# Kernel tuning notes

Hardware: AMD Instinct MI355X
Metric: run time of the kernel (lower is better)

The kernel has to match this reference:

```python
import jax, jax.numpy as jnp
import numpy as np

FP8_MAX = 448.0  # float8_e4m3fn max
EPS = 1e-6


def _rms_norm(x, w):
    # x: [T, H], w: [H]
    var = jnp.mean(x * x, axis=-1, keepdims=True)
    return x * jax.lax.rsqrt(var + EPS) * w


def _fused_add_rms_norm(x, resid, w):
    r = x + resid
    return _rms_norm(r, w), r


def _fp8_linear(y, W):
    # dynamic per-token activation quant + per-tensor weight quant, fp8 e4m3
    s = jnp.maximum(jnp.max(jnp.abs(y), axis=-1, keepdims=True) / FP8_MAX, 1e-12)  # [T,1]
    qx = jnp.clip(y / s, -FP8_MAX, FP8_MAX).astype(jnp.float8_e4m3fn).astype(jnp.float32)
    ws = jnp.maximum(jnp.max(jnp.abs(W)) / FP8_MAX, 1e-12)  # scalar
    qw = jnp.clip(W / ws, -FP8_MAX, FP8_MAX).astype(jnp.float8_e4m3fn).astype(jnp.float32)
    # out = dequant(qx) @ dequant(qw).T = (qx @ qw.T) * s * ws ; W is [out, in]
    return (qx @ qw.T) * (s * ws)


def setup_inputs() -> dict:
    key = jax.random.key(0)
    ks = jax.random.split(key, 8)
    H, T = 4096, 4096
    x = jax.random.normal(ks[0], (T, H), dtype=jnp.float32)
    nw0 = 1.0 + 0.02 * jax.random.normal(ks[1], (H,), dtype=jnp.float32)
    nw1 = 1.0 + 0.02 * jax.random.normal(ks[2], (H,), dtype=jnp.float32)
    nw2 = 1.0 + 0.02 * jax.random.normal(ks[3], (H,), dtype=jnp.float32)
    nw3 = 1.0 + 0.02 * jax.random.normal(ks[4], (H,), dtype=jnp.float32)
    W0 = 0.02 * jax.random.normal(ks[5], (H, H), dtype=jnp.float32)
    W1 = 0.02 * jax.random.normal(ks[6], (H, H), dtype=jnp.float32)
    W2 = 0.02 * jax.random.normal(ks[7], (H, H), dtype=jnp.float32)
    return {"x": x, "nw0": nw0, "nw1": nw1, "nw2": nw2, "nw3": nw3,
            "W0": W0, "W1": W1, "W2": W2}


def reference(x, nw0, nw1, nw2, nw3, W0, W1, W2):
    x = jax.nn.relu(x)
    resid = x
    y = _rms_norm(x, nw0)
    x2 = _fp8_linear(y, W0)
    y2, resid = _fused_add_rms_norm(x2, resid, nw1)
    x3 = _fp8_linear(y2, W1)
    y3, resid = _fused_add_rms_norm(x3, resid, nw2)
    x4 = _fp8_linear(y3, W2)
    y4, resid = _fused_add_rms_norm(x4, resid, nw3)
    return y4
```

## Files before the change

### kernel.cpp

```cpp
#include <hip/hip_runtime.h>
#include <cstdint>
#include <cstddef>

#define AS1 __attribute__((address_space(1)))
#define AS3 __attribute__((address_space(3)))

typedef __attribute__((ext_vector_type(4))) float f32x4;
typedef __attribute__((ext_vector_type(16))) float f32x16;
typedef __attribute__((ext_vector_type(4))) int i32x4;
typedef __attribute__((ext_vector_type(8))) int i32x8;

constexpr int HD = 4096;
constexpr float FP8MAX = 448.0f;

__device__ inline uint32_t pack4_fp8(float a, float b, float c, float d) {
    int v = 0;
    v = __builtin_amdgcn_cvt_pk_fp8_f32(a, b, v, false);
    v = __builtin_amdgcn_cvt_pk_fp8_f32(c, d, v, true);
    return (uint32_t)v;
}

__device__ inline float clipmul(float y, float rcs) {
    float t = y * rcs;
    t = fminf(t, FP8MAX);
    t = fmaxf(t, -FP8MAX);
    return t;
}

__device__ inline uint32_t quant4(float4 v, float rcs) {
    return pack4_fp8(clipmul(v.x, rcs), clipmul(v.y, rcs),
                     clipmul(v.z, rcs), clipmul(v.w, rcs));
}

__device__ inline float max4(float4 v) {
    return fmaxf(fmaxf(fabsf(v.x), fabsf(v.y)), fmaxf(fabsf(v.z), fabsf(v.w)));
}

__global__ __launch_bounds__(256) void w_absmax(const float* __restrict__ W0,
                                                const float* __restrict__ W1,
                                                const float* __restrict__ W2,
                                                uint32_t* __restrict__ wmax) {
    __shared__ float red[4];
    const float* W = (blockIdx.z == 0) ? W0 : (blockIdx.z == 1 ? W1 : W2);
    const float4* W4 = (const float4*)W;
    const int n4 = HD * HD / 4;
    float m = 0.f;
    for (int i = blockIdx.x * blockDim.x + threadIdx.x; i < n4; i += gridDim.x * blockDim.x) {
        m = fmaxf(m, max4(W4[i]));
    }
#pragma unroll
    for (int i = 32; i > 0; i >>= 1) m = fmaxf(m, __shfl_xor(m, i, 64));
    if ((threadIdx.x & 63) == 0) red[threadIdx.x >> 6] = m;
    __syncthreads();
    if (threadIdx.x == 0) {
        m = fmaxf(fmaxf(red[0], red[1]), fmaxf(red[2], red[3]));
        atomicMax((unsigned int*)(wmax + blockIdx.z), __float_as_uint(m));
    }
}

__global__ __launch_bounds__(256) void w_absmax1(const float* __restrict__ W,
                                                 uint32_t* __restrict__ slot) {
    __shared__ float red[4];
    const float4* W4 = (const float4*)W;
    const int stride = 2048 * 256;
    int i = blockIdx.x * 256 + threadIdx.x;
    float a0 = 0.f, a1 = 0.f, a2 = 0.f, a3 = 0.f;
#pragma unroll
    for (int it = 0; it < 2; it++) {
        float4 v0 = W4[i];
        float4 v1 = W4[i + stride];
        float4 v2 = W4[i + 2 * stride];
        float4 v3 = W4[i + 3 * stride];
        a0 = fmaxf(a0, max4(v0));
        a1 = fmaxf(a1, max4(v1));
        a2 = fmaxf(a2, max4(v2));
        a3 = fmaxf(a3, max4(v3));
        i += 4 * stride;
    }
    float m = fmaxf(fmaxf(a0, a1), fmaxf(a2, a3));
#pragma unroll
    for (int s = 32; s > 0; s >>= 1) m = fmaxf(m, __shfl_xor(m, s, 64));
    if ((threadIdx.x & 63) == 0) red[threadIdx.x >> 6] = m;
    __syncthreads();
    if (threadIdx.x == 0) {
        m = fmaxf(fmaxf(red[0], red[1]), fmaxf(red[2], red[3]));
        atomicMax((unsigned int*)slot, __float_as_uint(m));
    }
}

__global__ __launch_bounds__(256) void w_quant(const float* __restrict__ W,
                                               const uint32_t* __restrict__ wmaxbits,
                                               uint32_t* __restrict__ qw) {
    const float rsw = 1.0f / fmaxf(__uint_as_float(*wmaxbits) / FP8MAX, 1e-12f);
    const int i = blockIdx.x * blockDim.x + threadIdx.x;
    qw[i] = quant4(((const float4*)W)[i], rsw);
}

__global__ __launch_bounds__(256) void fused_rms(const float* __restrict__ xin,
                                                 const float* __restrict__ addin,
                                                 float* __restrict__ resid_out,
                                                 const float* __restrict__ nw,
                                                 uint32_t* __restrict__ qx,
                                                 float* __restrict__ srow,
                                                 float* __restrict__ yout,
                                                 const int mode,
                                                 const float* __restrict__ Wq,
                                                 const uint32_t* __restrict__ wqmaxbits,
                                                 uint32_t* __restrict__ qwout,
                                                 const float* __restrict__ Wa1,
                                                 const float* __restrict__ Wa2,
                                                 uint32_t* __restrict__ wmaxbase) {
    const int tid = threadIdx.x;
    __shared__ float reds[4];
    __shared__ float redm[4];

    if (blockIdx.x >= 8192) {
        const int b = blockIdx.x - 8192;
        const float* W = (b < 512) ? Wa1 : Wa2;
        uint32_t* slot = wmaxbase + ((b < 512) ? 1 : 2);
        const int bb = b & 511;
        const float4* W4 = (const float4*)W;
        const int stride = 512 * 256;
        int i = bb * 256 + tid;
        float a0 = 0.f, a1 = 0.f, a2 = 0.f, a3 = 0.f;
#pragma unroll
        for (int it = 0; it < 8; it++) {
            float4 v0 = W4[i];
            float4 v1 = W4[i + stride];
            float4 v2 = W4[i + 2 * stride];
            float4 v3 = W4[i + 3 * stride];
            a0 = fmaxf(a0, max4(v0));
            a1 = fmaxf(a1, max4(v1));
            a2 = fmaxf(a2, max4(v2));
            a3 = fmaxf(a3, max4(v3));
            i += 4 * stride;
        }
        float m = fmaxf(fmaxf(a0, a1), fmaxf(a2, a3));
#pragma unroll
        for (int s = 32; s > 0; s >>= 1) m = fmaxf(m, __shfl_xor(m, s, 64));
        if ((tid & 63) == 0) reds[tid >> 6] = m;
        __syncthreads();
        if (tid == 0) {
            m = fmaxf(fmaxf(reds[0], reds[1]), fmaxf(reds[2], reds[3]));
            atomicMax((unsigned int*)slot, __float_as_uint(m));
        }
        return;
    }

    if (blockIdx.x >= 4096) {
        const float rsw = 1.0f / fmaxf(__uint_as_float(*wqmaxbits) / FP8MAX, 1e-12f);
        const float4* W4 = (const float4*)Wq;
        int i = (blockIdx.x - 4096) * 256 + tid;
#pragma unroll
        for (int it = 0; it < 4; it++, i += 4096 * 256)
            qwout[i] = quant4(W4[i], rsw);
        return;
    }

    const int row = blockIdx.x;
    const size_t base = (size_t)row * HD;
    const float4* xr = (const float4*)(xin + base);
    const float4* nw4 = (const float4*)nw;

    float4 v[4], w[4];
    float ss = 0.f, pm = 0.f;
    if (mode == 0) {
#pragma unroll
        for (int j = 0; j < 4; j++) {
            float4 t = xr[tid + j * 256];
            w[j] = nw4[tid + j * 256];
            t.x = fmaxf(t.x, 0.f); t.y = fmaxf(t.y, 0.f);
            t.z = fmaxf(t.z, 0.f); t.w = fmaxf(t.w, 0.f);
            v[j] = t;
            ss += t.x * t.x + t.y * t.y + t.z * t.z + t.w * t.w;
            pm = fmaxf(pm, fmaxf(fmaxf(fabsf(t.x * w[j].x), fabsf(t.y * w[j].y)),
                                 fmaxf(fabsf(t.z * w[j].z), fabsf(t.w * w[j].w))));
        }
    } else {
        const float4* ar = (const float4*)(addin + base);
#pragma unroll
        for (int j = 0; j < 4; j++) {
            float4 t = xr[tid + j * 256];
            float4 a = ar[tid + j * 256];
            w[j] = nw4[tid + j * 256];
            t.x += a.x; t.y += a.y; t.z += a.z; t.w += a.w;
            v[j] = t;
            ss += t.x * t.x + t.y * t.y + t.z * t.z + t.w * t.w;
            pm = fmaxf(pm, fmaxf(fmaxf(fabsf(t.x * w[j].x), fabsf(t.y * w[j].y)),
                                 fmaxf(fabsf(t.z * w[j].z), fabsf(t.w * w[j].w))));
        }
    }
    if (resid_out) {
        float4* ro = (float4*)(resid_out + base);
#pragma unroll
        for (int j = 0; j < 4; j++) ro[tid + j * 256] = v[j];
    }

#pragma unroll
    for (int i = 32; i > 0; i >>= 1) {
        ss += __shfl_xor(ss, i, 64);
        pm = fmaxf(pm, __shfl_xor(pm, i, 64));
    }
    if ((tid & 63) == 0) { reds[tid >> 6] = ss; redm[tid >> 6] = pm; }
    __syncthreads();
    ss = (reds[0] + reds[1]) + (reds[2] + reds[3]);
    pm = fmaxf(fmaxf(redm[0], redm[1]), fmaxf(redm[2], redm[3]));

    const float rs = 1.0f / sqrtf(ss / (float)HD + 1e-6f);

    if (mode == 2) {
        float4* yo = (float4*)(yout + base);
#pragma unroll
        for (int j = 0; j < 4; j++) {
            float4 t;
            t.x = (v[j].x * rs) * w[j].x; t.y = (v[j].y * rs) * w[j].y;
            t.z = (v[j].z * rs) * w[j].z; t.w = (v[j].w * rs) * w[j].w;
            yo[tid + j * 256] = t;
        }
        return;
    }

    const float amax = pm * rs;
    const float s = fmaxf(amax / FP8MAX, 1e-12f);
    const float rcs = 1.0f / s;
    if (tid == 0) srow[row] = s;
    uint32_t* qr = qx + base / 4;
#pragma unroll
    for (int j = 0; j < 4; j++) {
        float4 t;
        t.x = (v[j].x * rs) * w[j].x; t.y = (v[j].y * rs) * w[j].y;
        t.z = (v[j].z * rs) * w[j].z; t.w = (v[j].w * rs) * w[j].w;
        qr[tid + j * 256] = quant4(t, rcs);
    }
}

typedef union { i32x8 v8; i32x4 v4[2]; } frag8;

__global__ __launch_bounds__(512, 2) void gemm_fp8mx(const uint8_t* __restrict__ qx,
                                                     const uint8_t* __restrict__ qw,
                                                     const float* __restrict__ srow,
                                                     const uint32_t* __restrict__ wmaxbits,
                                                     float* __restrict__ out) {
    __shared__ i32x4 AsL[2][2][1024];
    __shared__ i32x4 BsL[2][2][1024];

    const int tid = threadIdx.x;
    const int wave = tid >> 6, lane = tid & 63;
    const int lr = lane & 31, lh = lane >> 5;
    const int m0 = blockIdx.y * 256, n0 = blockIdx.x * 256;
    const int wm = (wave >> 2) * 128, wn = (wave & 3) * 64;

    const int str = tid >> 2;
    const int skg = (tid & 3) ^ ((str >> 1) & 3);
    const size_t srcA = (size_t)(m0 + str) * HD + (size_t)(skg * 16);
    const size_t srcB = (size_t)(n0 + str) * HD + (size_t)(skg * 16);

    f32x16 acc[4][2];
#pragma unroll
    for (int i = 0; i < 4; i++)
#pragma unroll
        for (int j = 0; j < 2; j++)
#pragma unroll
            for (int e = 0; e < 16; e++) acc[i][j][e] = 0.f;

    frag8 af0, af1, af2, af3, bf0, bf1;

#define STAGE_U(gp, soff, larr, koff) do {                                              \
    __builtin_amdgcn_global_load_lds((const AS1 void*)((gp) + (soff) + (size_t)(koff)), \
                                     (AS3 void*)((larr) + tid), 16, 0, 0);              \
    __builtin_amdgcn_global_load_lds((const AS1 void*)((gp) + (soff) + (size_t)(koff) + 128u * HD), \
                                     (AS3 void*)((larr) + 512 + tid), 16, 0, 0);        \
} while (0)

#define READ_F(dst, rbase, larr) do {                 \
    const int r_ = (rbase);                           \
    const i32x4* p_ = (larr) + r_ * 4;                \
    const int sw_ = (r_ >> 1) & 3;                    \
    dst.v4[0] = p_[(lh * 2) ^ sw_];                   \
    dst.v4[1] = p_[(lh * 2 + 1) ^ sw_];               \
} while (0)

#define MFMA1(a_, b_, i_, j_)                                                            \
    acc[i_][j_] = __builtin_amdgcn_mfma_scale_f32_32x32x64_f8f6f4(                       \
        (a_).v8, (b_).v8, acc[i_][j_], 0, 0, 0, 0x7F7F7F7Fu, 0, 0x7F7F7F7Fu)

#define HALF(bR, kh) do {                                           \
    READ_F(af0, wm + lr,      &AsL[bR][kh][0]);                     \
    READ_F(af1, wm + 32 + lr, &AsL[bR][kh][0]);                     \
    READ_F(bf0, wn + lr,      &BsL[bR][kh][0]);                     \
    READ_F(bf1, wn + 32 + lr, &BsL[bR][kh][0]);                     \
    READ_F(af2, wm + 64 + lr, &AsL[bR][kh][0]);                     \
    READ_F(af3, wm + 96 + lr, &AsL[bR][kh][0]);                     \
    __builtin_amdgcn_s_setprio(1);                                  \
    MFMA1(af0, bf0, 0, 0); MFMA1(af0, bf1, 0, 1);                   \
    MFMA1(af1, bf0, 1, 0); MFMA1(af1, bf1, 1, 1);                   \
    MFMA1(af2, bf0, 2, 0); MFMA1(af2, bf1, 2, 1);                   \
    MFMA1(af3, bf0, 3, 0); MFMA1(af3, bf1, 3, 1);                   \
    __builtin_amdgcn_s_setprio(0);                                  \
} while (0)

#define KTILE(bR, bS, knext) do {                                   \
    STAGE_U(qx, srcA, &AsL[bS][0][0], (knext));                     \
    STAGE_U(qx, srcA, &AsL[bS][1][0], (knext) + 64);                \
    STAGE_U(qw, srcB, &BsL[bS][0][0], (knext));                     \
    STAGE_U(qw, srcB, &BsL[bS][1][0], (knext) + 64);                \
    HALF(bR, 0);                                                    \
    HALF(bR, 1);                                                    \
    asm volatile("s_waitcnt vmcnt(0)" ::: "memory");                \
    __builtin_amdgcn_s_barrier();                                   \
    __builtin_amdgcn_sched_barrier(0);                              \
} while (0)

    STAGE_U(qx, srcA, &AsL[0][0][0], 0);
    STAGE_U(qx, srcA, &AsL[0][1][0], 64);
    STAGE_U(qw, srcB, &BsL[0][0][0], 0);
    STAGE_U(qw, srcB, &BsL[0][1][0], 64);
    asm volatile("s_waitcnt vmcnt(0)" ::: "memory");
    __builtin_amdgcn_s_barrier();
    __builtin_amdgcn_sched_barrier(0);

#pragma unroll 1
    for (int kt = 0; kt < 32; kt += 2) {
        KTILE(0, 1, (kt + 1) * 128);
        KTILE(1, 0, ((kt + 2) & 31) * 128);
    }

    const float wsc = fmaxf(__uint_as_float(*wmaxbits) / FP8MAX, 1e-12f);
#pragma unroll
    for (int i = 0; i < 4; i++) {
#pragma unroll
        for (int reg = 0; reg < 16; reg++) {
            const int row = (reg & 3) + 8 * (reg >> 2) + 4 * lh;
            const int m = m0 + wm + i * 32 + row;
            const float sv = srow[m] * wsc;
            float* orow = out + (size_t)m * HD + n0 + wn + lr;
#pragma unroll
            for (int j = 0; j < 2; j++)
                orow[j * 32] = acc[i][j][reg] * sv;
        }
    }
#undef KTILE
#undef HALF
#undef MFMA1
#undef READ_F
#undef STAGE_U
}

extern "C" void kernel_launch(void* const* d_in, const int* in_sizes, int n_in,
                              void* d_out, int out_size, void* d_ws, size_t ws_size,
                              hipStream_t stream) {
    const float* x   = (const float*)d_in[0];
    const float* nw0 = (const float*)d_in[1];
    const float* nw1 = (const float*)d_in[2];
    const float* nw2 = (const float*)d_in[3];
    const float* nw3 = (const float*)d_in[4];
    const float* W0  = (const float*)d_in[5];
    const float* W1  = (const float*)d_in[6];
    const float* W2  = (const float*)d_in[7];
    float* out = (float*)d_out;

    char* ws = (char*)d_ws;
    const size_t MB = 1024 * 1024;
    float* x2 = out;

    const bool overlap = ws_size >= 118 * MB;

    if (overlap) {
        float*    resid = (float*)(ws);
        uint32_t* qx    = (uint32_t*)(ws + 64 * MB);
        uint32_t* qwA   = (uint32_t*)(ws + 80 * MB);
        uint32_t* qwB   = (uint32_t*)(ws + 96 * MB);
        float*    srow  = (float*)(ws + 112 * MB);
        uint32_t* wmax  = (uint32_t*)(ws + 112 * MB + 16384);

        hipMemsetAsync(wmax, 0, 12, stream);
        hipLaunchKernelGGL(w_absmax1, dim3(2048), dim3(256), 0, stream, W0, wmax + 0);

        hipLaunchKernelGGL(fused_rms, dim3(9216), dim3(256), 0, stream,
                           x, (const float*)nullptr, resid, nw0, qx, srow, (float*)nullptr, 0,
                           W0, wmax + 0, qwA, W1, W2, wmax);
        hipLaunchKernelGGL(gemm_fp8mx, dim3(16, 16), dim3(512), 0, stream,
                           (const uint8_t*)qx, (const uint8_t*)qwA, srow, wmax + 0, x2);
        hipLaunchKernelGGL(fused_rms, dim3(8192), dim3(256), 0, stream,
                           x2, (const float*)resid, resid, nw1, qx, srow, (float*)nullptr, 1,
                           W1, wmax + 1, qwB,
                           (const float*)nullptr, (const float*)nullptr, (uint32_t*)nullptr);
        hipLaunchKernelGGL(gemm_fp8mx, dim3(16, 16), dim3(512), 0, stream,
                           (const uint8_t*)qx, (const uint8_t*)qwB, srow, wmax + 1, x2);
        hipLaunchKernelGGL(fused_rms, dim3(8192), dim3(256), 0, stream,
                           x2, (const float*)resid, resid, nw2, qx, srow, (float*)nullptr, 1,
                           W2, wmax + 2, qwA,
                           (const float*)nullptr, (const float*)nullptr, (uint32_t*)nullptr);
        hipLaunchKernelGGL(gemm_fp8mx, dim3(16, 16), dim3(512), 0, stream,
                           (const uint8_t*)qx, (const uint8_t*)qwA, srow, wmax + 2, x2);
        hipLaunchKernelGGL(fused_rms, dim3(4096), dim3(256), 0, stream,
                           x2, (const float*)resid, (float*)nullptr, nw3,
                           (uint32_t*)nullptr, (float*)nullptr, out, 2,
                           (const float*)nullptr, (const uint32_t*)nullptr, (uint32_t*)nullptr,
                           (const float*)nullptr, (const float*)nullptr, (uint32_t*)nullptr);
    } else {
        float*    resid = (float*)(ws);
        uint32_t* qx    = (uint32_t*)(ws + 64 * MB);
        uint32_t* qw    = (uint32_t*)(ws + 80 * MB);
        float*    srow  = (float*)(ws + 96 * MB);
        uint32_t* wmax  = (uint32_t*)(ws + 96 * MB + 16384);

        hipMemsetAsync(wmax, 0, 12, stream);
        hipLaunchKernelGGL(w_absmax, dim3(1024, 1, 3), dim3(256), 0, stream, W0, W1, W2, wmax);
        hipLaunchKernelGGL(fused_rms, dim3(4096), dim3(256), 0, stream,
                           x, (const float*)nullptr, resid, nw0, qx, srow, (float*)nullptr, 0,
                           (const float*)nullptr, (const uint32_t*)nullptr, (uint32_t*)nullptr,
                           (const float*)nullptr, (const float*)nullptr, (uint32_t*)nullptr);
        const float* Ws[3]  = {W0, W1, W2};
        const float* nws[3] = {nw1, nw2, nw3};
        for (int l = 0; l < 3; l++) {
            hipLaunchKernelGGL(w_quant, dim3(HD * HD / 4 / 256), dim3(256), 0, stream,
                               Ws[l], wmax + l, qw);
            hipLaunchKernelGGL(gemm_fp8mx, dim3(16, 16), dim3(512), 0, stream,
                               (const uint8_t*)qx, (const uint8_t*)qw, srow, wmax + l, x2);
            if (l < 2) {
                hipLaunchKernelGGL(fused_rms, dim3(4096), dim3(256), 0, stream,
                                   x2, (const float*)resid, resid, nws[l], qx, srow,
                                   (float*)nullptr, 1,
                                   (const float*)nullptr, (const uint32_t*)nullptr, (uint32_t*)nullptr,
                                   (const float*)nullptr, (const float*)nullptr, (uint32_t*)nullptr);
            } else {
                hipLaunchKernelGGL(fused_rms, dim3(4096), dim3(256), 0, stream,
                                   x2, (const float*)resid, (float*)nullptr, nws[l],
                                   (uint32_t*)nullptr, (float*)nullptr, out, 2,
                                   (const float*)nullptr, (const uint32_t*)nullptr, (uint32_t*)nullptr,
                                   (const float*)nullptr, (const float*)nullptr, (uint32_t*)nullptr);
            }
        }
    }
}
```

Measured before the change: 625.7 us.

## Fuse residual add into GEMM epilogue and interleave staging with MFMA halves

New measurement: 629.6 us. No clear change (+0.6%).

```diff
diff --git a/kernel.cpp b/kernel.cpp
--- a/kernel.cpp
+++ b/kernel.cpp
@@ -97,7 +97,6 @@
 }
 
 __global__ __launch_bounds__(256) void fused_rms(const float* __restrict__ xin,
-                                                 const float* __restrict__ addin,
                                                  float* __restrict__ resid_out,
                                                  const float* __restrict__ nw,
                                                  uint32_t* __restrict__ qx,
@@ -177,13 +176,10 @@
                                  fmaxf(fabsf(t.z * w[j].z), fabsf(t.w * w[j].w))));
         }
     } else {
-        const float4* ar = (const float4*)(addin + base);
 #pragma unroll
         for (int j = 0; j < 4; j++) {
             float4 t = xr[tid + j * 256];
-            float4 a = ar[tid + j * 256];
             w[j] = nw4[tid + j * 256];
-            t.x += a.x; t.y += a.y; t.z += a.z; t.w += a.w;
             v[j] = t;
             ss += t.x * t.x + t.y * t.y + t.z * t.z + t.w * t.w;
             pm = fmaxf(pm, fmaxf(fmaxf(fabsf(t.x * w[j].x), fabsf(t.y * w[j].y)),
@@ -240,7 +236,7 @@
                                                      const uint8_t* __restrict__ qw,
                                                      const float* __restrict__ srow,
                                                      const uint32_t* __restrict__ wmaxbits,
-                                                     float* __restrict__ out) {
+                                                     float* resid) {
     __shared__ i32x4 AsL[2][2][1024];
     __shared__ i32x4 BsL[2][2][1024];
 
@@ -284,40 +280,45 @@
     acc[i_][j_] = __builtin_amdgcn_mfma_scale_f32_32x32x64_f8f6f4(                       \
         (a_).v8, (b_).v8, acc[i_][j_], 0, 0, 0, 0x7F7F7F7Fu, 0, 0x7F7F7F7Fu)
 
-#define HALF(bR, kh) do {                                           \
+#define MFMA4(a0_, a1_, r0_, r1_) do {               \
+    __builtin_amdgcn_s_setprio(1);                   \
+    MFMA1(a0_, bf0, r0_, 0);                         \
+    MFMA1(a0_, bf1, r0_, 1);                         \
+    MFMA1(a1_, bf0, r1_, 0);                         \
+    MFMA1(a1_, bf1, r1_, 1);                         \
+    __builtin_amdgcn_s_setprio(0);                   \
+} while (0)
+
+#define KHALF(bR, bS, kh, knext) do {                               \
+                             \
     READ_F(af0, wm + lr,      &AsL[bR][kh][0]);                     \
     READ_F(af1, wm + 32 + lr, &AsL[bR][kh][0]);                     \
     READ_F(bf0, wn + lr,      &BsL[bR][kh][0]);                     \
     READ_F(bf1, wn + 32 + lr, &BsL[bR][kh][0]);                     \
     READ_F(af2, wm + 64 + lr, &AsL[bR][kh][0]);                     \
     READ_F(af3, wm + 96 + lr, &AsL[bR][kh][0]);                     \
-    __builtin_amdgcn_s_setprio(1);                                  \
-    MFMA1(af0, bf0, 0, 0); MFMA1(af0, bf1, 0, 1);                   \
-    MFMA1(af1, bf0, 1, 0); MFMA1(af1, bf1, 1, 1);                   \
-    MFMA1(af2, bf0, 2, 0); MFMA1(af2, bf1, 2, 1);                   \
-    MFMA1(af3, bf0, 3, 0); MFMA1(af3, bf1, 3, 1);                   \
-    __builtin_amdgcn_s_setprio(0);                                  \
+    STAGE_U(qx, srcA, &AsL[bS][kh][0], (knext));                    \
+    __builtin_amdgcn_s_barrier();                                   \
+    MFMA4(af0, af1, 0, 1);                                          \
+    __builtin_amdgcn_s_barrier();                                   \
+    STAGE_U(qw, srcB, &BsL[bS][kh][0], (knext));                    \
+    __builtin_amdgcn_s_barrier();                                   \
+    MFMA4(af2, af3, 2, 3);                                          \
+    asm volatile("s_waitcnt vmcnt(4)" ::: "memory");                \
+    __builtin_amdgcn_s_barrier();                                   \
 } while (0)
 
 #define KTILE(bR, bS, knext) do {                                   \
-    STAGE_U(qx, srcA, &AsL[bS][0][0], (knext));                     \
-    STAGE_U(qx, srcA, &AsL[bS][1][0], (knext) + 64);                \
-    STAGE_U(qw, srcB, &BsL[bS][0][0], (knext));                     \
-    STAGE_U(qw, srcB, &BsL[bS][1][0], (knext) + 64);                \
-    HALF(bR, 0);                                                    \
-    HALF(bR, 1);                                                    \
-    asm volatile("s_waitcnt vmcnt(0)" ::: "memory");                \
-    __builtin_amdgcn_s_barrier();                                   \
-    __builtin_amdgcn_sched_barrier(0);                              \
+    KHALF(bR, bS, 0, (knext));                                      \
+    KHALF(bR, bS, 1, (knext) + 64);                                 \
 } while (0)
 
     STAGE_U(qx, srcA, &AsL[0][0][0], 0);
+    STAGE_U(qw, srcB, &BsL[0][0][0], 0);
     STAGE_U(qx, srcA, &AsL[0][1][0], 64);
-    STAGE_U(qw, srcB, &BsL[0][0][0], 0);
     STAGE_U(qw, srcB, &BsL[0][1][0], 64);
-    asm volatile("s_waitcnt vmcnt(0)" ::: "memory");
+    asm volatile("s_waitcnt vmcnt(4)" ::: "memory");
     __builtin_amdgcn_s_barrier();
-    __builtin_amdgcn_sched_barrier(0);
 
 #pragma unroll 1
     for (int kt = 0; kt < 32; kt += 2) {
@@ -333,14 +334,15 @@
             const int row = (reg & 3) + 8 * (reg >> 2) + 4 * lh;
             const int m = m0 + wm + i * 32 + row;
             const float sv = srow[m] * wsc;
-            float* orow = out + (size_t)m * HD + n0 + wn + lr;
+            float* orow = resid + (size_t)m * HD + n0 + wn + lr;
 #pragma unroll
             for (int j = 0; j < 2; j++)
-                orow[j * 32] = acc[i][j][reg] * sv;
+                orow[j * 32] = acc[i][j][reg] * sv + orow[j * 32];
         }
     }
 #undef KTILE
-#undef HALF
+#undef KHALF
+#undef MFMA4
 #undef MFMA1
 #undef READ_F
 #undef STAGE_U
@@ -361,7 +363,6 @@
 
     char* ws = (char*)d_ws;
     const size_t MB = 1024 * 1024;
-    float* x2 = out;
 
     const bool overlap = ws_size >= 118 * MB;
 
@@ -377,24 +378,24 @@
         hipLaunchKernelGGL(w_absmax1, dim3(2048), dim3(256), 0, stream, W0, wmax + 0);
 
         hipLaunchKernelGGL(fused_rms, dim3(9216), dim3(256), 0, stream,
-                           x, (const float*)nullptr, resid, nw0, qx, srow, (float*)nullptr, 0,
+                           x, resid, nw0, qx, srow, (float*)nullptr, 0,
                            W0, wmax + 0, qwA, W1, W2, wmax);
         hipLaunchKernelGGL(gemm_fp8mx, dim3(16, 16), dim3(512), 0, stream,
-                           (const uint8_t*)qx, (const uint8_t*)qwA, srow, wmax + 0, x2);
+                           (const uint8_t*)qx, (const uint8_t*)qwA, srow, wmax + 0, resid);
         hipLaunchKernelGGL(fused_rms, dim3(8192), dim3(256), 0, stream,
-                           x2, (const float*)resid, resid, nw1, qx, srow, (float*)nullptr, 1,
+                           resid, (float*)nullptr, nw1, qx, srow, (float*)nullptr, 1,
                            W1, wmax + 1, qwB,
                            (const float*)nullptr, (const float*)nullptr, (uint32_t*)nullptr);
         hipLaunchKernelGGL(gemm_fp8mx, dim3(16, 16), dim3(512), 0, stream,
-                           (const uint8_t*)qx, (const uint8_t*)qwB, srow, wmax + 1, x2);
+                           (const uint8_t*)qx, (const uint8_t*)qwB, srow, wmax + 1, resid);
         hipLaunchKernelGGL(fused_rms, dim3(8192), dim3(256), 0, stream,
-                           x2, (const float*)resid, resid, nw2, qx, srow, (float*)nullptr, 1,
+                           resid, (float*)nullptr, nw2, qx, srow, (float*)nullptr, 1,
                            W2, wmax + 2, qwA,
                            (const float*)nullptr, (const float*)nullptr, (uint32_t*)nullptr);
         hipLaunchKernelGGL(gemm_fp8mx, dim3(16, 16), dim3(512), 0, stream,
-                           (const uint8_t*)qx, (const uint8_t*)qwA, srow, wmax + 2, x2);
+                           (const uint8_t*)qx, (const uint8_t*)qwA, srow, wmax + 2, resid);
         hipLaunchKernelGGL(fused_rms, dim3(4096), dim3(256), 0, stream,
-                           x2, (const float*)resid, (float*)nullptr, nw3,
+                           resid, (float*)nullptr, nw3,
                            (uint32_t*)nullptr, (float*)nullptr, out, 2,
                            (const float*)nullptr, (const uint32_t*)nullptr, (uint32_t*)nullptr,
                            (const float*)nullptr, (const float*)nullptr, (uint32_t*)nullptr);
@@ -408,7 +409,7 @@
         hipMemsetAsync(wmax, 0, 12, stream);
         hipLaunchKernelGGL(w_absmax, dim3(1024, 1, 3), dim3(256), 0, stream, W0, W1, W2, wmax);
         hipLaunchKernelGGL(fused_rms, dim3(4096), dim3(256), 0, stream,
-                           x, (const float*)nullptr, resid, nw0, qx, srow, (float*)nullptr, 0,
+                           x, resid, nw0, qx, srow, (float*)nullptr, 0,
                            (const float*)nullptr, (const uint32_t*)nullptr, (uint32_t*)nullptr,
                            (const float*)nullptr, (const float*)nullptr, (uint32_t*)nullptr);
         const float* Ws[3]  = {W0, W1, W2};
@@ -417,16 +418,16 @@
             hipLaunchKernelGGL(w_quant, dim3(HD * HD / 4 / 256), dim3(256), 0, stream,
                                Ws[l], wmax + l, qw);
             hipLaunchKernelGGL(gemm_fp8mx, dim3(16, 16), dim3(512), 0, stream,
-                               (const uint8_t*)qx, (const uint8_t*)qw, srow, wmax + l, x2);
+                               (const uint8_t*)qx, (const uint8_t*)qw, srow, wmax + l, resid);
             if (l < 2) {
                 hipLaunchKernelGGL(fused_rms, dim3(4096), dim3(256), 0, stream,
-                                   x2, (const float*)resid, resid, nws[l], qx, srow,
+                                   resid, (float*)nullptr, nws[l], qx, srow,
                                    (float*)nullptr, 1,
                                    (const float*)nullptr, (const uint32_t*)nullptr, (uint32_t*)nullptr,
                                    (const float*)nullptr, (const float*)nullptr, (uint32_t*)nullptr);
             } else {
                 hipLaunchKernelGGL(fused_rms, dim3(4096), dim3(256), 0, stream,
-                                   x2, (const float*)resid, (float*)nullptr, nws[l],
+                                   resid, (float*)nullptr, nws[l],
                                    (uint32_t*)nullptr, (float*)nullptr, out, 2,
                                    (const float*)nullptr, (const uint32_t*)nullptr, (uint32_t*)nullptr,
                                    (const float*)nullptr, (const float*)nullptr, (uint32_t*)nullptr);
```
